# Kernel optimization log

Measured on AMD Instinct MI355X. Metric: run time of the kernel, lower is better.

The kernel has to match this reference:

```python
import jax, jax.numpy as jnp
import numpy as np
from jax import lax

B, C, H, W, P = 16, 256, 64, 64, 4
EPS = 1e-5


def setup_inputs() -> dict:
    key = jax.random.key(0)
    ks = jax.random.split(key, 16)
    s = 0.05
    d = {
        'rgb': jax.random.normal(ks[0], (B, C, H, W), jnp.float32),
        'th': jax.random.normal(ks[1], (B, C, H, W), jnp.float32),
        'q_w': jax.random.normal(ks[2], (C, C), jnp.float32) * s,
        'q_b': jax.random.normal(ks[3], (C,), jnp.float32) * s,
        'kvr_w': jax.random.normal(ks[4], (2 * C, C), jnp.float32) * s,
        'kvr_b': jax.random.normal(ks[5], (2 * C,), jnp.float32) * s,
        'kvt_w': jax.random.normal(ks[6], (2 * C, C), jnp.float32) * s,
        'kvt_b': jax.random.normal(ks[7], (2 * C,), jnp.float32) * s,
        'offr_w': jax.random.normal(ks[8], (2 * P, C, 3, 3), jnp.float32) * s,
        'offr_b': jax.random.normal(ks[9], (2 * P,), jnp.float32) * s,
        'offt_w': jax.random.normal(ks[10], (2 * P, C, 3, 3), jnp.float32) * s,
        'offt_b': jax.random.normal(ks[11], (2 * P,), jnp.float32) * s,
        'out_w': jax.random.normal(ks[12], (C, 2 * C), jnp.float32) * s,
        'out_b': jax.random.normal(ks[13], (C,), jnp.float32) * s,
        'gamma': jnp.ones((C,), jnp.float32),
        'beta': jnp.zeros((C,), jnp.float32),
    }
    return d


def conv1x1(x, w, b):
    # x: [B,Ci,H,W], w: [Co,Ci] -> [B,Co,H,W]
    return jnp.einsum('bchw,oc->bohw', x, w) + b[None, :, None, None]


def conv3x3(x, w, b):
    y = lax.conv_general_dilated(x, w, (1, 1), 'SAME',
                                 dimension_numbers=('NCHW', 'OIHW', 'NCHW'))
    return y + b[None, :, None, None]


def deform_sample(feat, offset):
    # feat: [B,C,H,W]; offset: [B,2P,H,W] (pixel-unit offsets, (x,y) pairs)
    Bs, Cs, Hs, Ws = feat.shape
    off = offset.reshape(Bs, -1, 2, Hs, Ws)  # [B,P,2,H,W]
    # base grid in [-1,1], align_corners=True convention
    gy = jnp.linspace(-1.0, 1.0, Hs)[None, None, :, None]
    gx = jnp.linspace(-1.0, 1.0, Ws)[None, None, None, :]
    grid_x = gx + off[:, :, 0] / (Ws / 2.0)  # [B,P,H,W]
    grid_y = gy + off[:, :, 1] / (Hs / 2.0)
    # normalized -> pixel coords (align_corners=True)
    x = (grid_x + 1.0) * (Ws - 1) / 2.0
    y = (grid_y + 1.0) * (Hs - 1) / 2.0
    x0 = jnp.floor(x)
    y0 = jnp.floor(y)
    wx = x - x0
    wy = y - y0
    feat_flat = feat.reshape(Bs, Cs, Hs * Ws)

    def corner(xi, yi, wgt):
        valid = (xi >= 0) & (xi < Ws) & (yi >= 0) & (yi < Hs)  # zeros padding
        xc = jnp.clip(xi, 0, Ws - 1).astype(jnp.int32)
        yc = jnp.clip(yi, 0, Hs - 1).astype(jnp.int32)
        idx = (yc * Ws + xc).reshape(Bs, 1, -1)  # [B,1,P*H*W]
        g = jnp.take_along_axis(feat_flat, jnp.broadcast_to(idx, (Bs, Cs, idx.shape[-1])), axis=2)
        g = g.reshape(Bs, Cs, -1, Hs, Ws)  # [B,C,P,H,W]
        w_eff = (wgt * valid.astype(feat.dtype))[:, None]  # [B,1,P,H,W]
        return g * w_eff

    x0i = x0.astype(jnp.int32)
    y0i = y0.astype(jnp.int32)
    out = (corner(x0i, y0i, (1 - wx) * (1 - wy))
           + corner(x0i + 1, y0i, wx * (1 - wy))
           + corner(x0i, y0i + 1, (1 - wx) * wy)
           + corner(x0i + 1, y0i + 1, wx * wy))
    return out.mean(axis=2)  # mean over P -> [B,C,H,W]


def batchnorm_train(x, gamma, beta):
    mu = x.mean(axis=(0, 2, 3), keepdims=True)
    var = x.var(axis=(0, 2, 3), keepdims=True)
    xn = (x - mu) * lax.rsqrt(var + EPS)
    return xn * gamma[None, :, None, None] + beta[None, :, None, None]


def reference(rgb, th, q_w, q_b, kvr_w, kvr_b, kvt_w, kvt_b,
              offr_w, offr_b, offt_w, offt_b, out_w, out_b, gamma, beta):
    q_rgb = conv1x1(rgb, q_w, q_b)
    q_th = conv1x1(th, q_w, q_b)
    kv_rgb = conv1x1(rgb, kvr_w, kvr_b)
    kv_th = conv1x1(th, kvt_w, kvt_b)
    v_rgb = kv_rgb[:, C:]  # k_rgb = kv_rgb[:, :C] is unused downstream
    v_th = kv_th[:, C:]
    off_rgb2th = conv3x3(th, offr_w, offr_b)
    off_th2rgb = conv3x3(rgb, offt_w, offt_b)
    v_rgb2th = deform_sample(v_rgb, off_rgb2th)
    v_th2rgb = deform_sample(v_th, off_th2rgb)
    attn_rgb = jax.nn.sigmoid(q_rgb) * v_th2rgb
    attn_th = jax.nn.sigmoid(q_th) * v_rgb2th
    fused = conv1x1(jnp.concatenate([attn_rgb, attn_th], axis=1), out_w, out_b)
    return batchnorm_train(fused + 0.5 * (rgb + th), gamma, beta)
```

## Files before the change

kernel.cpp:

```cpp
#include <hip/hip_runtime.h>

typedef __bf16 bf16x8 __attribute__((ext_vector_type(8)));
typedef float  f32x4  __attribute__((ext_vector_type(4)));

constexpr int Bn = 16, Cn = 256, Hn = 64, Wn = 64, HWn = 64 * 64;
constexpr int Ntot = Bn * HWn;

#define DEV static __device__ __forceinline__

DEV unsigned short f2bf(float f) {
  unsigned u = __builtin_bit_cast(unsigned, f);
  u += 0x7fffu + ((u >> 16) & 1u);
  return (unsigned short)(u >> 16);
}
DEV float bf2f(unsigned short s) {
  unsigned u = ((unsigned)s) << 16;
  return __builtin_bit_cast(float, u);
}
DEV bf16x8 asbf(uint4 u) { return __builtin_bit_cast(bf16x8, u); }

__global__ void k_prep(const float* qw, const float* kvrw, const float* kvtw,
                       const float* offrw, const float* offtw, const float* outw,
                       unsigned short* Aqv, unsigned short* Aoff, unsigned short* Aout) {
  int idx = blockIdx.x * 256 + threadIdx.x;
  if (idx < 2 * 512 * 256) {
    int t = idx >> 17; int r = idx & 131071; int o = r >> 8; int c = r & 255;
    float v = (o < 256) ? qw[o * 256 + c] : (t ? kvtw[o * 256 + c] : kvrw[o * 256 + c]);
    Aqv[idx] = f2bf(v);
    return;
  }
  idx -= 2 * 512 * 256;
  if (idx < 2 * 16 * 2304) {
    int t = idx / 36864; int r = idx % 36864;
    int o = r / 2304; int rc = r % 2304; int tap = rc >> 8; int c = rc & 255;
    const float* w = t ? offtw : offrw;
    float v = (o < 8) ? w[(o * 256 + c) * 9 + tap] : 0.f;
    Aoff[idx] = f2bf(v);
    return;
  }
  idx -= 2 * 16 * 2304;
  if (idx < 256 * 512) {
    int seg = idx >> 11, o = (idx >> 3) & 255, e = idx & 7;
    Aout[idx] = f2bf(outw[o * 512 + seg * 8 + e]);
  }
}

__global__ void k_transpose(const float* rgb, const float* th, unsigned short* xT) {
  int bi = blockIdx.x;
  int ct = bi & 3;
  int nt = (bi >> 2) & 63;
  int b  = (bi >> 8) & 15;
  int t  = bi >> 12;
  const float* src = t ? th : rgb;
  int c0 = ct * 64, n0 = nt * 64;
  __shared__ float tile[64][65];
  int tid = threadIdx.x;
  int nl = tid & 63, cg = tid >> 6;
#pragma unroll
  for (int i = 0; i < 16; i++) {
    int c = cg * 16 + i;
    tile[c][nl] = src[(size_t)(b * 256 + c0 + c) * HWn + n0 + nl];
  }
  __syncthreads();
  int pr = tid >> 2, sg = tid & 3;
  unsigned short tmp[16];
#pragma unroll
  for (int j = 0; j < 16; j++) tmp[j] = f2bf(tile[sg * 16 + j][pr]);
  unsigned short* dst = xT + (size_t)t * Ntot * 256 +
                        (size_t)(b * HWn + n0 + pr) * 256 + c0 + sg * 16;
  *(uint4*)(dst)     = *(const uint4*)(tmp);
  *(uint4*)(dst + 8) = *(const uint4*)(tmp + 8);
}

__global__ __launch_bounds__(512, 2) void k_qv(
    const unsigned short* Aqv, const unsigned short* xT,
    const float* qb, const float* kvrb, const float* kvtb,
    unsigned short* qs, unsigned short* vv) {
  __shared__ unsigned short smem[32768];
  int t  = blockIdx.z;
  int mt = blockIdx.y;
  int nt = blockIdx.x;
  int swznt = ((nt & 7) << 6) | (nt >> 3);
  int o0 = mt * 128;
  int n0 = swznt * 128;
  int tid = threadIdx.x;
  const unsigned short* Aq = Aqv + t * 512 * 256;
  const unsigned short* Xg = xT + (size_t)t * Ntot * 256 + (size_t)n0 * 256;

  auto stage = [&](int kb, int bb) {
    unsigned short* As = smem + bb * 8192;
    unsigned short* Xs = smem + 16384 + bb * 8192;
#pragma unroll
    for (int i = 0; i < 2; i++) {
      int cid = tid + i * 512;
      int row = cid >> 3, seg = cid & 7;
      int ss = seg ^ (row & 7);
      *(uint4*)(&As[row * 64 + seg * 8]) =
          *(const uint4*)(Aq + (size_t)(o0 + row) * 256 + kb * 64 + ss * 8);
    }
#pragma unroll
    for (int i = 0; i < 2; i++) {
      int cid = tid + i * 512;
      int row = cid >> 3, seg = cid & 7;
      int ss = seg ^ (row & 7);
      *(uint4*)(&Xs[row * 64 + seg * 8]) =
          *(const uint4*)(Xg + (size_t)row * 256 + kb * 64 + ss * 8);
    }
  };

  int w = __builtin_amdgcn_readfirstlane(tid >> 6);
  int lane = tid & 63;
  int wo = w & 1, wn = w >> 1;
  int r16 = lane & 15, q4 = lane >> 4;

  f32x4 acc[4][2];
#pragma unroll
  for (int a = 0; a < 4; a++) { acc[a][0] = f32x4{0.f,0.f,0.f,0.f}; acc[a][1] = f32x4{0.f,0.f,0.f,0.f}; }

  stage(0, 0);
  __syncthreads();
#pragma unroll
  for (int kb = 0; kb < 4; kb++) {
    if (kb < 3) stage(kb + 1, (kb + 1) & 1);
    const unsigned short* As = smem + (kb & 1) * 8192;
    const unsigned short* Xs = smem + 16384 + (kb & 1) * 8192;
#pragma unroll
    for (int ks = 0; ks < 2; ks++) {
      uint4 af[4], bfr[2];
#pragma unroll
      for (int oi = 0; oi < 4; oi++) {
        int row = wo * 64 + oi * 16 + r16;
        int seg = (ks * 4 + q4) ^ (row & 7);
        af[oi] = *(const uint4*)(&As[row * 64 + seg * 8]);
      }
#pragma unroll
      for (int ni = 0; ni < 2; ni++) {
        int row = wn * 32 + ni * 16 + r16;
        int seg = (ks * 4 + q4) ^ (row & 7);
        bfr[ni] = *(const uint4*)(&Xs[row * 64 + seg * 8]);
      }
#pragma unroll
      for (int oi = 0; oi < 4; oi++)
#pragma unroll
        for (int ni = 0; ni < 2; ni++)
          acc[oi][ni] = __builtin_amdgcn_mfma_f32_16x16x32_bf16(
              asbf(af[oi]), asbf(bfr[ni]), acc[oi][ni], 0, 0, 0);
    }
    __syncthreads();
  }

  bool isq = (mt < 2);
  const float* bias = isq ? qb : (t ? kvtb : kvrb);
  float4 bv[4];
#pragma unroll
  for (int oi = 0; oi < 4; oi++)
    bv[oi] = *(const float4*)(&bias[o0 + wo * 64 + oi * 16 + q4 * 4]);
#pragma unroll
  for (int oi = 0; oi < 4; oi++) {
    int ol = wo * 64 + oi * 16 + q4 * 4;
#pragma unroll
    for (int ni = 0; ni < 2; ni++) {
      int nl = wn * 32 + ni * 16 + r16;
      unsigned short pk[4];
#pragma unroll
      for (int j = 0; j < 4; j++) {
        float val = acc[oi][ni][j] + ((const float*)&bv[oi])[j];
        if (isq) val = 1.f / (1.f + __expf(-val));
        pk[j] = f2bf(val);
      }
      *(uint2*)(&smem[nl * 132 + ol]) = *(const uint2*)(pk);
    }
  }
  __syncthreads();
  unsigned short* outp = (isq ? qs : vv) + (size_t)t * Ntot * 256 + (mt & 1) * 128;
#pragma unroll
  for (int pass = 0; pass < 4; pass++) {
    int nl = pass * 32 + (tid >> 4);
    int c  = tid & 15;
    uint4 vq = *(const uint4*)(&smem[nl * 132 + c * 8]);
    *(uint4*)(outp + (size_t)(n0 + nl) * 256 + c * 8) = vq;
  }
}

__global__ __launch_bounds__(256, 4) void k_off(
    const unsigned short* Aoff, const unsigned short* xT,
    const float* offrb, const float* offtb, float* offo) {
  __shared__ unsigned short Alds[9 * 8 * 264 + 264];
  int t  = blockIdx.y;
  int bh = blockIdx.x;
  int swz = ((bh & 7) << 7) | (bh >> 3);
  int b = swz >> 6, h = swz & 63;
  int tid = threadIdx.x;
  const unsigned short* Aw = Aoff + t * 36864;

#pragma unroll
  for (int i = 0; i < 9; i++) {
    int cid = tid + i * 256;
    int o = cid / 288;
    int rem = cid - o * 288;
    int tap = rem >> 5, cg = rem & 31;
    uint4 v = *(const uint4*)(Aw + o * 2304 + tap * 256 + cg * 8);
    *(uint4*)(&Alds[(tap * 8 + o) * 264 + cg * 8]) = v;
  }
  if (tid < 33) {
    uint4 z; z.x = 0; z.y = 0; z.z = 0; z.w = 0;
    *(uint4*)(&Alds[19008 + tid * 8]) = z;
  }
  __syncthreads();

  int lane = tid & 63, w = tid >> 6;
  int r16 = lane & 15, q4 = lane >> 4;
  int wl = w * 16 + r16;
  const unsigned short* xin = xT + (size_t)(t ? 0 : 1) * Ntot * 256;
  int zbase = 19008 + q4 * 8;
  int abase = r16 * 264 + q4 * 8;
  bool rowok = (r16 < 8);

  f32x4 acc = {0.f, 0.f, 0.f, 0.f};
  uint4 bufA[8], bufB[8];

#define LOADT(buf, tap) {                                                      \
    int dy = (tap) / 3 - 1, dx = (tap) % 3 - 1;                                \
    int hh = h + dy, ww = wl + dx;                                             \
    bool ok = (hh >= 0 && hh < 64 && ww >= 0 && ww < 64);                      \
    int hc = hh < 0 ? 0 : (hh > 63 ? 63 : hh);                                 \
    int wc = ww < 0 ? 0 : (ww > 63 ? 63 : ww);                                 \
    const unsigned short* p =                                                  \
        xin + (size_t)(((b * 64 + hc) * 64 + wc) * 256) + q4 * 8;              \
    _Pragma("unroll") for (int ks = 0; ks < 8; ks++) {                         \
      uint4 v = *(const uint4*)(p + ks * 32);                                  \
      if (!ok) { v.x = 0; v.y = 0; v.z = 0; v.w = 0; }                         \
      buf[ks] = v;                                                             \
    } }

#define COMPT(buf, tap) {                                                      \
    _Pragma("unroll") for (int ks = 0; ks < 8; ks++) {                         \
      int aofs = rowok ? ((tap) * 8 * 264 + abase + ks * 32) : (zbase + ks * 32); \
      uint4 af = *(const uint4*)(&Alds[aofs]);                                 \
      acc = __builtin_amdgcn_mfma_f32_16x16x32_bf16(asbf(af), asbf(buf[ks]),   \
                                                    acc, 0, 0, 0);             \
    } }

  LOADT(bufA, 0)
  LOADT(bufB, 1)
  COMPT(bufA, 0)
  LOADT(bufA, 2)
  COMPT(bufB, 1)
  LOADT(bufB, 3)
  COMPT(bufA, 2)
  LOADT(bufA, 4)
  COMPT(bufB, 3)
  LOADT(bufB, 5)
  COMPT(bufA, 4)
  LOADT(bufA, 6)
  COMPT(bufB, 5)
  LOADT(bufB, 7)
  COMPT(bufA, 6)
  LOADT(bufA, 8)
  COMPT(bufB, 7)
  COMPT(bufA, 8)
#undef LOADT
#undef COMPT

  if (lane < 32) {
    const float* ob = t ? offtb : offrb;
    int n = (b * 64 + h) * 64 + wl;
    float4 r;
    r.x = acc[0] + ob[q4 * 4 + 0];
    r.y = acc[1] + ob[q4 * 4 + 1];
    r.z = acc[2] + ob[q4 * 4 + 2];
    r.w = acc[3] + ob[q4 * 4 + 3];
    *(float4*)(offo + (size_t)t * Ntot * 8 + (size_t)n * 8 + q4 * 4) = r;
  }
}

DEV void addrw(int px, int h, int b, int c0, float dx, float dy,
               int* coff, float* cwgt) {
  float xf = (float)px + dx * (63.f / 64.f);
  float yf = (float)h  + dy * (63.f / 64.f);
  float x0f = floorf(xf), y0f = floorf(yf);
  float wx = xf - x0f, wy = yf - y0f;
  int x0 = (int)x0f, y0 = (int)y0f;
#pragma unroll
  for (int c = 0; c < 4; c++) {
    int cy2 = c >> 1, cx2 = c & 1;
    int ix = x0 + cx2, iy = y0 + cy2;
    bool ok = (ix >= 0 && ix < 64 && iy >= 0 && iy < 64);
    int ixc = ix < 0 ? 0 : (ix > 63 ? 63 : ix);
    int iyc = iy < 0 ? 0 : (iy > 63 ? 63 : iy);
    float wgt = (cx2 ? wx : 1.f - wx) * (cy2 ? wy : 1.f - wy);
    cwgt[c] = ok ? wgt : 0.f;
    coff[c] = ((b * 64 + iyc) * 64 + ixc) * 256 + c0;
  }
}

__global__ __launch_bounds__(512, 4) void k_fuse(
    const unsigned short* qs, const unsigned short* vv, const float* offo,
    const unsigned short* Apk, const float* outb,
    const float* rgb, const float* th, float* dout, float* partial) {
  __shared__ unsigned short cc[16 * 512];
  __shared__ float bstat[256][2];
  int tid = threadIdx.x;
  int bi  = blockIdx.x;
  int swz = ((bi & 7) << 9) | (bi >> 3);
  int b = swz >> 8;
  int h = (swz >> 2) & 63;
  int px0 = (swz & 3) * 16;
  if (tid < 256) { bstat[tid][0] = 0.f; bstat[tid][1] = 0.f; }

  {
    int pxL = tid >> 5, chunk = tid & 31;
    int px = px0 + pxL;
    int n = (b * 64 + h) * 64 + px;
    int c0 = chunk * 8;
    int sw = pxL & 7;
#pragma unroll
    for (int pass = 0; pass < 2; pass++) {
      const unsigned short* vsrc = vv + (size_t)(pass ? 0 : 1) * Ntot * 256;
      const float* offp = offo + (size_t)(pass ? 0 : 1) * Ntot * 8 + (size_t)n * 8;
      const unsigned short* qsrc = qs + (size_t)(pass ? 1 : 0) * Ntot * 256 + (size_t)n * 256;
      uint4  q0  = *(const uint4*)(qsrc + c0);
      float4 of0 = *(const float4*)(offp);
      float4 of1 = *(const float4*)(offp + 4);
      float acc[8];
#pragma unroll
      for (int i = 0; i < 8; i++) acc[i] = 0.f;

      int   coffA[4], coffB[4];
      float cwgtA[4], cwgtB[4];
      uint4 bufA[4], bufB[4];
#define LOADG(buf, co) { _Pragma("unroll") for (int c2 = 0; c2 < 4; c2++)      \
        buf[c2] = *(const uint4*)(vsrc + co[c2]); }
#define FMAG(buf, cw) { _Pragma("unroll") for (int c2 = 0; c2 < 4; c2++) {     \
        const unsigned short* a0 = (const unsigned short*)&buf[c2];            \
        float wv2 = cw[c2];                                                    \
        _Pragma("unroll") for (int e = 0; e < 8; e++)                          \
          acc[e] += wv2 * bf2f(a0[e]); } }
      addrw(px, h, b, c0, of0.x, of0.y, coffA, cwgtA);
      LOADG(bufA, coffA)
      addrw(px, h, b, c0, of0.z, of0.w, coffB, cwgtB);
      LOADG(bufB, coffB)
      FMAG(bufA, cwgtA)
      addrw(px, h, b, c0, of1.x, of1.y, coffA, cwgtA);
      LOADG(bufA, coffA)
      FMAG(bufB, cwgtB)
      addrw(px, h, b, c0, of1.z, of1.w, coffB, cwgtB);
      LOADG(bufB, coffB)
      FMAG(bufA, cwgtA)
      FMAG(bufB, cwgtB)
#undef LOADG
#undef FMAG
      const unsigned short* qp0 = (const unsigned short*)&q0;
      unsigned short pk[8];
#pragma unroll
      for (int e = 0; e < 8; e++) pk[e] = f2bf(0.25f * acc[e] * bf2f(qp0[e]));
      *(uint4*)(&cc[pxL * 512 + ((pass * 32 + chunk) ^ sw) * 8]) = *(const uint4*)(pk);
    }
  }
  __syncthreads();

  int lane = tid & 63, wv = tid >> 6;
  int r16 = lane & 15, q4 = lane >> 4;
  f32x4 acc2[2];
  acc2[0] = f32x4{0.f, 0.f, 0.f, 0.f};
  acc2[1] = f32x4{0.f, 0.f, 0.f, 0.f};
#pragma unroll
  for (int kst = 0; kst < 16; kst++) {
    int slot = (kst * 4 + q4) ^ (r16 & 7);
    uint4 bfr = *(const uint4*)(&cc[r16 * 512 + slot * 8]);
#pragma unroll
    for (int oi = 0; oi < 2; oi++) {
      int o = wv * 32 + oi * 16 + r16;
      uint4 a = *(const uint4*)(Apk + (size_t)((kst * 4 + q4) * 256 + o) * 8);
      acc2[oi] = __builtin_amdgcn_mfma_f32_16x16x32_bf16(asbf(a), asbf(bfr), acc2[oi], 0, 0, 0);
    }
  }
#pragma unroll
  for (int oi = 0; oi < 2; oi++) {
    int ob = wv * 32 + oi * 16 + q4 * 4;
#pragma unroll
    for (int j = 0; j < 4; j++) {
      int o = ob + j;
      int hw = h * 64 + px0 + r16;
      size_t gidx = (size_t)(b * 256 + o) * HWn + hw;
      float val = acc2[oi][j] + outb[o] + 0.5f * (rgb[gidx] + th[gidx]);
      dout[gidx] = val;
      float s1 = val, s2 = val * val;
#pragma unroll
      for (int m = 1; m < 16; m <<= 1) {
        s1 += __shfl_xor(s1, m, 16);
        s2 += __shfl_xor(s2, m, 16);
      }
      if (r16 == 0) { atomicAdd(&bstat[o][0], s1); atomicAdd(&bstat[o][1], s2); }
    }
  }
  __syncthreads();
  if (tid < 256) {
    partial[(size_t)bi * 512 + tid]       = bstat[tid][0];
    partial[(size_t)bi * 512 + 256 + tid] = bstat[tid][1];
  }
}

__global__ void k_stats(const float* partial, const float* gamma, const float* beta,
                        float* sstats) {
  int c = blockIdx.x, tid = threadIdx.x;
  float s1 = 0.f, s2 = 0.f;
  for (int i = tid; i < 4096; i += 256) {
    s1 += partial[(size_t)i * 512 + c];
    s2 += partial[(size_t)i * 512 + 256 + c];
  }
  __shared__ float r1[256], r2[256];
  r1[tid] = s1; r2[tid] = s2;
  __syncthreads();
  for (int st = 128; st > 0; st >>= 1) {
    if (tid < st) { r1[tid] += r1[tid + st]; r2[tid] += r2[tid + st]; }
    __syncthreads();
  }
  if (tid == 0) {
    float mean = r1[0] / 65536.f;
    float var  = r2[0] / 65536.f - mean * mean;
    float scale = gamma[c] / sqrtf(var + 1e-5f);
    sstats[c]       = scale;
    sstats[256 + c] = beta[c] - mean * scale;
  }
}

__global__ void k_bn(float* dout, const float* sstats) {
  int idx = blockIdx.x * 256 + threadIdx.x;
  size_t base = (size_t)idx * 4;
  int c = (int)((base >> 12) & 255);
  float4 v = *(float4*)(dout + base);
  float sc = sstats[c], sh = sstats[256 + c];
  v.x = v.x * sc + sh; v.y = v.y * sc + sh;
  v.z = v.z * sc + sh; v.w = v.w * sc + sh;
  *(float4*)(dout + base) = v;
}

extern "C" void kernel_launch(void* const* d_in, const int* in_sizes, int n_in,
                              void* d_out, int out_size, void* d_ws, size_t ws_size,
                              hipStream_t stream) {
  const float* rgb   = (const float*)d_in[0];
  const float* th    = (const float*)d_in[1];
  const float* qw    = (const float*)d_in[2];
  const float* qb    = (const float*)d_in[3];
  const float* kvrw  = (const float*)d_in[4];
  const float* kvrb  = (const float*)d_in[5];
  const float* kvtw  = (const float*)d_in[6];
  const float* kvtb  = (const float*)d_in[7];
  const float* offrw = (const float*)d_in[8];
  const float* offrb = (const float*)d_in[9];
  const float* offtw = (const float*)d_in[10];
  const float* offtb = (const float*)d_in[11];
  const float* outw  = (const float*)d_in[12];
  const float* outb  = (const float*)d_in[13];
  const float* gamma = (const float*)d_in[14];
  const float* beta  = (const float*)d_in[15];
  float* dout = (float*)d_out;

  unsigned short* xT   = (unsigned short*)d_ws;
  unsigned short* qsb  = xT  + (size_t)2 * Ntot * 256;
  unsigned short* vvb  = qsb + (size_t)2 * Ntot * 256;
  float* offo          = (float*)(vvb + (size_t)2 * Ntot * 256);
  unsigned short* Aqv  = (unsigned short*)(offo + (size_t)2 * Ntot * 8);
  unsigned short* Aoff = Aqv + 2 * 512 * 256;
  unsigned short* Aout = Aoff + 2 * 16 * 2304;
  float* partial       = (float*)(Aout + 256 * 512);
  float* sstats        = partial + (size_t)4096 * 512;

  k_prep<<<1824, 256, 0, stream>>>(qw, kvrw, kvtw, offrw, offtw, outw, Aqv, Aoff, Aout);
  k_transpose<<<8192, 256, 0, stream>>>(rgb, th, xT);
  k_qv<<<dim3(512, 4, 2), 512, 0, stream>>>(Aqv, xT, qb, kvrb, kvtb, qsb, vvb);
  k_off<<<dim3(1024, 2), 256, 0, stream>>>(Aoff, xT, offrb, offtb, offo);
  k_fuse<<<4096, 512, 0, stream>>>(qsb, vvb, offo, Aout, outb, rgb, th, dout, partial);
  k_stats<<<256, 256, 0, stream>>>(partial, gamma, beta, sstats);
  k_bn<<<16384, 256, 0, stream>>>(dout, sstats);
}
```

Baseline: 400.9 us.

## Move BN statistics out of fuse kernel into dout re-read; packed bf16 FMA

Drops the per-block shared-memory atomics, shuffle reductions and partial-sum writes from the fused attention/output-conv kernel. The stats kernel now re-reads the full 64 MB output tensor to compute per-channel sums. The deformable-sampling accumulation also switches to packed two-wide FMAs with bit-shift bf16 unpacking and a hardware packed bf16 convert. This trades a heavier, extra global read in k_stats for a lighter fuse kernel with less synchronisation.

```diff
diff --git a/kernel.cpp b/kernel.cpp
--- a/kernel.cpp
+++ b/kernel.cpp
@@ -2,6 +2,7 @@
 
 typedef __bf16 bf16x8 __attribute__((ext_vector_type(8)));
 typedef float  f32x4  __attribute__((ext_vector_type(4)));
+typedef float  f32x2  __attribute__((ext_vector_type(2)));
 
 constexpr int Bn = 16, Cn = 256, Hn = 64, Wn = 64, HWn = 64 * 64;
 constexpr int Ntot = Bn * HWn;
@@ -297,16 +298,14 @@
 __global__ __launch_bounds__(512, 4) void k_fuse(
     const unsigned short* qs, const unsigned short* vv, const float* offo,
     const unsigned short* Apk, const float* outb,
-    const float* rgb, const float* th, float* dout, float* partial) {
+    const float* rgb, const float* th, float* dout) {
   __shared__ unsigned short cc[16 * 512];
-  __shared__ float bstat[256][2];
   int tid = threadIdx.x;
   int bi  = blockIdx.x;
   int swz = ((bi & 7) << 9) | (bi >> 3);
   int b = swz >> 8;
   int h = (swz >> 2) & 63;
   int px0 = (swz & 3) * 16;
-  if (tid < 256) { bstat[tid][0] = 0.f; bstat[tid][1] = 0.f; }
 
   {
     int pxL = tid >> 5, chunk = tid & 31;
@@ -322,9 +321,9 @@
       uint4  q0  = *(const uint4*)(qsrc + c0);
       float4 of0 = *(const float4*)(offp);
       float4 of1 = *(const float4*)(offp + 4);
-      float acc[8];
-#pragma unroll
-      for (int i = 0; i < 8; i++) acc[i] = 0.f;
+      f32x2 accv[4];
+#pragma unroll
+      for (int i = 0; i < 4; i++) accv[i] = f32x2{0.f, 0.f};
 
       int   coffA[4], coffB[4];
       float cwgtA[4], cwgtB[4];
@@ -332,10 +331,12 @@
 #define LOADG(buf, co) { _Pragma("unroll") for (int c2 = 0; c2 < 4; c2++)      \
         buf[c2] = *(const uint4*)(vsrc + co[c2]); }
 #define FMAG(buf, cw) { _Pragma("unroll") for (int c2 = 0; c2 < 4; c2++) {     \
-        const unsigned short* a0 = (const unsigned short*)&buf[c2];            \
-        float wv2 = cw[c2];                                                    \
-        _Pragma("unroll") for (int e = 0; e < 8; e++)                          \
-          acc[e] += wv2 * bf2f(a0[e]); } }
+        f32x2 w2 = {cw[c2], cw[c2]};                                           \
+        const unsigned* uu = (const unsigned*)&buf[c2];                        \
+        _Pragma("unroll") for (int j2 = 0; j2 < 4; j2++) {                     \
+          f32x2 v2 = { __builtin_bit_cast(float, uu[j2] << 16),                \
+                       __builtin_bit_cast(float, uu[j2] & 0xffff0000u) };      \
+          accv[j2] = __builtin_elementwise_fma(v2, w2, accv[j2]); } } }
       addrw(px, h, b, c0, of0.x, of0.y, coffA, cwgtA);
       LOADG(bufA, coffA)
       addrw(px, h, b, c0, of0.z, of0.w, coffB, cwgtB);
@@ -350,11 +351,20 @@
       FMAG(bufB, cwgtB)
 #undef LOADG
 #undef FMAG
-      const unsigned short* qp0 = (const unsigned short*)&q0;
-      unsigned short pk[8];
-#pragma unroll
-      for (int e = 0; e < 8; e++) pk[e] = f2bf(0.25f * acc[e] * bf2f(qp0[e]));
-      *(uint4*)(&cc[pxL * 512 + ((pass * 32 + chunk) ^ sw) * 8]) = *(const uint4*)(pk);
+      const unsigned* qu = (const unsigned*)&q0;
+      unsigned pk2[4];
+#pragma unroll
+      for (int j2 = 0; j2 < 4; j2++) {
+        f32x2 q2 = { __builtin_bit_cast(float, qu[j2] << 16),
+                     __builtin_bit_cast(float, qu[j2] & 0xffff0000u) };
+        f32x2 r2 = accv[j2] * q2 * 0.25f;
+        unsigned ow;
+        asm("v_cvt_pk_bf16_f32 %0, %1, %2" : "=v"(ow) : "v"(r2.x), "v"(r2.y));
+        pk2[j2] = ow;
+      }
+      uint4 pkv;
+      pkv.x = pk2[0]; pkv.y = pk2[1]; pkv.z = pk2[2]; pkv.w = pk2[3];
+      *(uint4*)(&cc[pxL * 512 + ((pass * 32 + chunk) ^ sw) * 8]) = pkv;
     }
   }
   __syncthreads();
@@ -383,31 +393,23 @@
       int o = ob + j;
       int hw = h * 64 + px0 + r16;
       size_t gidx = (size_t)(b * 256 + o) * HWn + hw;
-      float val = acc2[oi][j] + outb[o] + 0.5f * (rgb[gidx] + th[gidx]);
-      dout[gidx] = val;
-      float s1 = val, s2 = val * val;
-#pragma unroll
-      for (int m = 1; m < 16; m <<= 1) {
-        s1 += __shfl_xor(s1, m, 16);
-        s2 += __shfl_xor(s2, m, 16);
-      }
-      if (r16 == 0) { atomicAdd(&bstat[o][0], s1); atomicAdd(&bstat[o][1], s2); }
-    }
-  }
-  __syncthreads();
-  if (tid < 256) {
-    partial[(size_t)bi * 512 + tid]       = bstat[tid][0];
-    partial[(size_t)bi * 512 + 256 + tid] = bstat[tid][1];
-  }
-}
-
-__global__ void k_stats(const float* partial, const float* gamma, const float* beta,
+      dout[gidx] = acc2[oi][j] + outb[o] + 0.5f * (rgb[gidx] + th[gidx]);
+    }
+  }
+}
+
+__global__ void k_stats(const float* dout, const float* gamma, const float* beta,
                         float* sstats) {
   int c = blockIdx.x, tid = threadIdx.x;
   float s1 = 0.f, s2 = 0.f;
-  for (int i = tid; i < 4096; i += 256) {
-    s1 += partial[(size_t)i * 512 + c];
-    s2 += partial[(size_t)i * 512 + 256 + c];
+#pragma unroll
+  for (int b2 = 0; b2 < 16; b2++) {
+    const float4* p = (const float4*)(dout + (size_t)(b2 * 256 + c) * HWn);
+    for (int i = tid; i < 1024; i += 256) {
+      float4 v = p[i];
+      s1 += v.x + v.y + v.z + v.w;
+      s2 += v.x * v.x + v.y * v.y + v.z * v.z + v.w * v.w;
+    }
   }
   __shared__ float r1[256], r2[256];
   r1[tid] = s1; r2[tid] = s2;
@@ -464,14 +466,13 @@
   unsigned short* Aqv  = (unsigned short*)(offo + (size_t)2 * Ntot * 8);
   unsigned short* Aoff = Aqv + 2 * 512 * 256;
   unsigned short* Aout = Aoff + 2 * 16 * 2304;
-  float* partial       = (float*)(Aout + 256 * 512);
-  float* sstats        = partial + (size_t)4096 * 512;
+  float* sstats        = (float*)(Aout + 256 * 512);
 
   k_prep<<<1824, 256, 0, stream>>>(qw, kvrw, kvtw, offrw, offtw, outw, Aqv, Aoff, Aout);
   k_transpose<<<8192, 256, 0, stream>>>(rgb, th, xT);
   k_qv<<<dim3(512, 4, 2), 512, 0, stream>>>(Aqv, xT, qb, kvrb, kvtb, qsb, vvb);
   k_off<<<dim3(1024, 2), 256, 0, stream>>>(Aoff, xT, offrb, offtb, offo);
-  k_fuse<<<4096, 512, 0, stream>>>(qsb, vvb, offo, Aout, outb, rgb, th, dout, partial);
-  k_stats<<<256, 256, 0, stream>>>(partial, gamma, beta, sstats);
+  k_fuse<<<4096, 512, 0, stream>>>(qsb, vvb, offo, Aout, outb, rgb, th, dout);
+  k_stats<<<256, 256, 0, stream>>>(dout, gamma, beta, sstats);
   k_bn<<<16384, 256, 0, stream>>>(dout, sstats);
 }
```

After: 405.4 us. About the same (+1.1%).
